# Performance work log

Hardware: AMD Instinct MI355X
Metric: run time of the kernel (lower is better)

The kernel has to match this reference:

```python
import jax, jax.numpy as jnp
import numpy as np

NUM_LAYERS = 3
NUM_NODES = 120000  # num_users + num_items
LATENT_DIM = 64
NUM_EDGES = 2000000


def setup_inputs() -> dict:
    key = jax.random.key(0)
    k1, k2 = jax.random.split(key)
    edge_index = jax.random.randint(k1, (2, NUM_EDGES), 0, NUM_NODES, dtype=jnp.int64 if jax.config.jax_enable_x64 else jnp.int32)
    # init_parameters: normal(std=0.1) for LightGCN
    emb_weight = jax.random.normal(k2, (NUM_NODES, LATENT_DIM), dtype=jnp.float32) * 0.1
    return {"edge_index": edge_index, "emb_weight": emb_weight}


def reference(edge_index, emb_weight):
    """RecSysGNN (model='LightGCN') forward. Returns (emb0, out)."""
    n = emb_weight.shape[0]
    src, dst = edge_index[0], edge_index[1]
    # degree of target nodes (degree(to_, x.size(0)))
    deg = jax.ops.segment_sum(jnp.ones(src.shape[0], dtype=emb_weight.dtype), dst, num_segments=n)
    deg_inv_sqrt = jnp.where(deg > 0, jax.lax.rsqrt(jnp.maximum(deg, 1.0)), 0.0)
    norm = deg_inv_sqrt[src] * deg_inv_sqrt[dst]  # [E]

    emb0 = emb_weight
    emb = emb0
    acc = emb0  # running sum of layer embeddings for final mean
    for _ in range(NUM_LAYERS):
        msg = norm[:, None] * emb[src]                      # [E, d] gather + scale
        emb = jax.ops.segment_sum(msg, dst, num_segments=n)  # scatter-add to targets
        acc = acc + emb
    out = acc / (NUM_LAYERS + 1)  # mean over stacked [emb0, emb1, ..., embL]
    return (emb0, out)
```

## Files before the change

kernel.cpp:

```cpp
#include <hip/hip_runtime.h>


#define DIM 64
#define BN 512
#define BSH 9
#define CHUNK 4096

typedef unsigned short u16;
typedef unsigned int u32;

static __device__ __forceinline__ float bf2f_lo(u32 p) { return __uint_as_float(p << 16); }
static __device__ __forceinline__ float bf2f_hi(u32 p) { return __uint_as_float(p & 0xffff0000u); }
static __device__ __forceinline__ u16 f2bf(float f) {
    unsigned u = __float_as_uint(f);
    return (u16)((u + 0x7fffu + ((u >> 16) & 1u)) >> 16);
}
static __device__ __forceinline__ u32 pack2(float a, float b) {
    return (u32)f2bf(a) | ((u32)f2bf(b) << 16);
}

__global__ void zero_cur(int* __restrict__ cursor) { cursor[threadIdx.x] = 0; }

__global__ void __launch_bounds__(512) c1_scatter(
        const int* __restrict__ src, const int* __restrict__ dst,
        int* __restrict__ cursor, u32* __restrict__ slab, int E, int CAP) {
    __shared__ u32 buf[CHUNK];
    __shared__ unsigned char bb[CHUNK];
    __shared__ int posb[256], startb[256], gbase[256];
    int w = blockIdx.x, tid = threadIdx.x;
    int lo = w * CHUNK, hi = min(lo + CHUNK, E);
    if (tid < 256) posb[tid] = 0;
    __syncthreads();
    for (int i = lo + tid; i < hi; i += 512) atomicAdd(&posb[dst[i] >> BSH], 1);
    __syncthreads();
    int x = 0;
    if (tid < 256) {
        x = posb[tid];
        gbase[tid] = x ? atomicAdd(cursor + tid, x) : 0;
    }
    __syncthreads();
    for (int off = 1; off < 256; off <<= 1) {
        int t = (tid >= off && tid < 256) ? posb[tid - off] : 0;
        __syncthreads();
        if (tid < 256) posb[tid] += t;
        __syncthreads();
    }
    if (tid < 256) startb[tid] = posb[tid] - x;
    __syncthreads();
    if (tid < 256) posb[tid] = startb[tid];
    __syncthreads();
    for (int i = lo + tid; i < hi; i += 512) {
        int d = dst[i], b = d >> BSH;
        int q = atomicAdd(&posb[b], 1);
        buf[q] = ((u32)src[i] << BSH) | (u32)(d & (BN - 1));
        bb[q] = (unsigned char)b;
    }
    __syncthreads();
    int n = hi - lo;
    for (int q = tid; q < n; q += 512) {
        int b = bb[q];
        slab[(size_t)b * CAP + gbase[b] + (q - startb[b])] = buf[q];
    }
}

__global__ void __launch_bounds__(512) c3_build(
        const u32* __restrict__ slab, const int* __restrict__ cursor,
        int* __restrict__ col, int2* __restrict__ row_se, float* __restrict__ dis,
        int N, int CAP, int NB) {
    __shared__ int cur[BN];
    __shared__ int ps[512];
    int b = blockIdx.x, tid = threadIdx.x;
    int xc = (tid < NB) ? cursor[tid] : 0;
    if (tid < 256) ps[tid] = xc;
    __syncthreads();
    for (int off = 1; off < 256; off <<= 1) {
        int t = (tid >= off && tid < 256) ? ps[tid - off] : 0;
        __syncthreads();
        if (tid < 256) ps[tid] += t;
        __syncthreads();
    }
    int lo  = b ? ps[b - 1] : 0;
    int cnt = cursor[b];
    __syncthreads();

    int nodeBase = b << BSH;
    int nLoc = min(BN, N - nodeBase);
    const u32* sp = slab + (size_t)b * CAP;
    cur[tid] = 0;
    __syncthreads();
    for (int i = tid; i < cnt; i += 512) atomicAdd(&cur[sp[i] & (BN - 1)], 1);
    __syncthreads();
    int c0 = cur[tid];
    ps[tid] = c0;
    __syncthreads();
    for (int off = 1; off < 512; off <<= 1) {
        int t = (tid >= off) ? ps[tid - off] : 0;
        __syncthreads();
        ps[tid] += t;
        __syncthreads();
    }
    int base = ps[tid] - c0;
    cur[tid] = base;
    if (tid < nLoc) {
        dis[nodeBase + tid] = c0 ? rsqrtf((float)c0) : 0.f;
        row_se[nodeBase + tid] = make_int2(lo + base, lo + base + c0);
    }
    __syncthreads();
    for (int i = tid; i < cnt; i += 512) {
        u32 v = sp[i];
        int q = atomicAdd(&cur[v & (BN - 1)], 1);
        col[lo + q] = (int)(v >> BSH);
    }
}

__global__ void cvt_copy(const float4* __restrict__ emb, const float* __restrict__ dis,
                         ushort4* __restrict__ e0b, float4* __restrict__ emb0_out, int n4) {
    int i = blockIdx.x * blockDim.x + threadIdx.x;
    if (i < n4) {
        float4 v = emb[i];
        float w = dis[i >> 4];
        ushort4 o;
        o.x = f2bf(w * v.x); o.y = f2bf(w * v.y);
        o.z = f2bf(w * v.z); o.w = f2bf(w * v.w);
        e0b[i] = o;
        emb0_out[i] = v;
    }
}

#define ACC4(P) { s0 += bf2f_lo((P).x); s1 += bf2f_hi((P).x);                  \
                  s2 += bf2f_lo((P).y); s3 += bf2f_hi((P).y); }

#define GATHER_BODY(CURTAB)                                                    \
    float s0 = 0.f, s1 = 0.f, s2 = 0.f, s3 = 0.f;                              \
    {                                                                          \
        int nfull = (end - start) >> 3;                                        \
        uint2 p0, p1, p2, p3;                                                  \
        if (nfull > 0) {                                                       \
            int j = start;                                                     \
            int a0 = col[j + g],     a1 = col[j + 2 + g];                      \
            int a2 = col[j + 4 + g], a3 = col[j + 6 + g];                      \
            p0 = *(const uint2*)((CURTAB) + (((size_t)a0) << 5) + 2 * d);      \
            p1 = *(const uint2*)((CURTAB) + (((size_t)a1) << 5) + 2 * d);      \
            p2 = *(const uint2*)((CURTAB) + (((size_t)a2) << 5) + 2 * d);      \
            p3 = *(const uint2*)((CURTAB) + (((size_t)a3) << 5) + 2 * d);      \
        }                                                                      \
        for (int r = 1; r < nfull; ++r) {                                      \
            int jn = start + 8 * r;                                            \
            int b0 = col[jn + g],     b1 = col[jn + 2 + g];                    \
            int b2 = col[jn + 4 + g], b3 = col[jn + 6 + g];                    \
            uint2 q0 = *(const uint2*)((CURTAB) + (((size_t)b0) << 5) + 2 * d);\
            uint2 q1 = *(const uint2*)((CURTAB) + (((size_t)b1) << 5) + 2 * d);\
            uint2 q2 = *(const uint2*)((CURTAB) + (((size_t)b2) << 5) + 2 * d);\
            uint2 q3 = *(const uint2*)((CURTAB) + (((size_t)b3) << 5) + 2 * d);\
            ACC4(p0) ACC4(p1) ACC4(p2) ACC4(p3)                                \
            p0 = q0; p1 = q1; p2 = q2; p3 = q3;                                \
        }                                                                      \
        if (nfull > 0) { ACC4(p0) ACC4(p1) ACC4(p2) ACC4(p3) }                 \
        int jt = start + 8 * nfull;                                            \
        if (jt < end) {                                                        \
            int endm1 = end - 1;                                               \
            _Pragma("unroll")                                                  \
            for (int k = 0; k < 4; ++k) {                                      \
                int e = jt + 2 * k + g;                                        \
                int c = col[min(e, endm1)];                                    \
                uint2 p = *(const uint2*)((CURTAB) + (((size_t)c) << 5) + 2 * d); \
                if (e >= end) { p.x = 0; p.y = 0; }                            \
                ACC4(p)                                                        \
            }                                                                  \
        }                                                                      \
    }                                                                          \
    s0 += __shfl_xor(s0, 16); s1 += __shfl_xor(s1, 16);                        \
    s2 += __shfl_xor(s2, 16); s3 += __shfl_xor(s3, 16);

__global__ void __launch_bounds__(256) gather_mid(
        const int2* __restrict__ row_se, const int* __restrict__ col,
        const float* __restrict__ dis, const u32* __restrict__ cur,
        u32* __restrict__ next, int N) {
    int t = blockIdx.x * blockDim.x + threadIdx.x;
    int pair = t >> 6, lane = t & 63;
    if (2 * pair >= N) return;
    int node = 2 * pair + (lane >> 5);
    int g = (lane >> 4) & 1, d = lane & 15;
    bool valid = node < N;
    int2 se = valid ? row_se[node] : make_int2(0, 0);
    int start = se.x, end = se.y;
    GATHER_BODY(cur)
    if (valid && g == 0) {
        float w = dis[node], ww = w * w;
        uint2 o;
        o.x = pack2(ww * s0, ww * s1);
        o.y = pack2(ww * s2, ww * s3);
        *(uint2*)(next + (((size_t)node) << 5) + 2 * d) = o;
    }
}

__global__ void __launch_bounds__(256) gather_final(
        const int2* __restrict__ row_se, const int* __restrict__ col,
        const float* __restrict__ dis, const u32* __restrict__ cur ,
        const u32* __restrict__ e1b, const float* __restrict__ emb0,
        float* __restrict__ out, int N) {
    int t = blockIdx.x * blockDim.x + threadIdx.x;
    int pair = t >> 6, lane = t & 63;
    if (2 * pair >= N) return;
    int node = 2 * pair + (lane >> 5);
    int g = (lane >> 4) & 1, d = lane & 15;
    bool valid = node < N;
    int2 se = valid ? row_se[node] : make_int2(0, 0);
    int start = se.x, end = se.y;
    GATHER_BODY(cur)
    if (valid && g == 0) {
        float w = dis[node];
        float inv = (w > 0.f) ? 1.0f / w : 0.f;
        size_t idx = (((size_t)node) << 5) + 2 * d;
        uint2 q1 = *(const uint2*)(e1b + idx);
        uint2 q2 = *(const uint2*)(cur + idx);
        float4 e0 = *(const float4*)(emb0 + 2 * idx);
        float4 r;
        r.x = 0.25f * (e0.x + (bf2f_lo(q1.x) + bf2f_lo(q2.x)) * inv + w * s0);
        r.y = 0.25f * (e0.y + (bf2f_hi(q1.x) + bf2f_hi(q2.x)) * inv + w * s1);
        r.z = 0.25f * (e0.z + (bf2f_lo(q1.y) + bf2f_lo(q2.y)) * inv + w * s2);
        r.w = 0.25f * (e0.w + (bf2f_hi(q1.y) + bf2f_hi(q2.y)) * inv + w * s3);
        *(float4*)(out + 2 * idx) = r;
    }
}

extern "C" void kernel_launch(void* const* d_in, const int* in_sizes, int n_in,
                              void* d_out, int out_size, void* d_ws, size_t ws_size,
                              hipStream_t stream) {
    const int*   edge  = (const int*)d_in[0];
    const float* emb_w = (const float*)d_in[1];
    const int E = in_sizes[0] / 2;
    const int N = in_sizes[1] / DIM;
    const int* src = edge;
    const int* dst = edge + E;

    const int NB  = (N + BN - 1) >> BSH;
    const int nCh = (E + CHUNK - 1) / CHUNK;
    const int CAP = (E / (NB > 0 ? NB : 1)) * 2;

    float* out_base = (float*)d_out;
    float* emb0_out = out_base;
    float* acc      = out_base + (size_t)N * DIM;

    float* dis       = (float*)d_ws;
    int2*  row_se    = (int2*)(dis + ((N + 1) & ~1));
    int*   cursor    = (int*)(row_se + N);
    int*   col       = cursor + 256;
    u32*   slab      = (u32*)(col + E);
    u16*   e0b       = (u16*)slab;
    u16*   e1b       = e0b + (size_t)N * DIM;

    const int n4    = N * DIM / 4;
    const int BLK   = 256;
    const int g4    = (n4 + BLK - 1) / BLK;
    const int PAIRS = (N + 1) / 2;
    const int gW    = (PAIRS * 64 + BLK - 1) / BLK;

    zero_cur<<<1, 256, 0, stream>>>(cursor);
    c1_scatter<<<nCh, 512, 0, stream>>>(src, dst, cursor, slab, E, CAP);
    c3_build<<<NB, 512, 0, stream>>>(slab, cursor, col, row_se, dis, N, CAP, NB);

    cvt_copy<<<g4, BLK, 0, stream>>>((const float4*)emb_w, dis,
                                     (ushort4*)e0b, (float4*)emb0_out, n4);

    gather_mid<<<gW, BLK, 0, stream>>>(row_se, col, dis, (const u32*)e0b, (u32*)e1b, N);
    gather_mid<<<gW, BLK, 0, stream>>>(row_se, col, dis, (const u32*)e1b, (u32*)e0b, N);
    gather_final<<<gW, BLK, 0, stream>>>(row_se, col, dis, (const u32*)e0b, (const u32*)e1b,
                                         emb_w, acc, N);
}
```

Before: 256.6 us.

## Split CSR rows into padded half-lists for vectorized column loads

The CSR build now stores each node's neighbour list as two interleaved halves, each padded to a multiple of four with zeros. This lets each half-wave in the gather read four column indices with a single 16-byte load instead of scalar strided loads. The layer-1 bf16 buffer is also moved into the output accumulator region with a 64-word row stride, freeing workspace, and gather_final reads it in place before overwriting it. The padding enlarges the col array and the build kernel does extra zero-filling work.

```diff
diff --git a/kernel.cpp b/kernel.cpp
--- a/kernel.cpp
+++ b/kernel.cpp
@@ -5,6 +5,7 @@
 #define BN 512
 #define BSH 9
 #define CHUNK 4096
+#define PADB 4096
 
 typedef unsigned short u16;
 typedef unsigned int u32;
@@ -68,6 +69,8 @@
         int* __restrict__ col, int2* __restrict__ row_se, float* __restrict__ dis,
         int N, int CAP, int NB) {
     __shared__ int cur[BN];
+    __shared__ int sAv[BN];
+    __shared__ int pAv[BN];
     __shared__ int ps[512];
     int b = blockIdx.x, tid = threadIdx.x;
     int xc = (tid < NB) ? cursor[tid] : 0;
@@ -79,9 +82,10 @@
         if (tid < 256) ps[tid] += t;
         __syncthreads();
     }
-    int lo  = b ? ps[b - 1] : 0;
+    int lo_raw = b ? ps[b - 1] : 0;
     int cnt = cursor[b];
     __syncthreads();
+    int lo_pad = ((lo_raw + 3) & ~3) + b * PADB;
 
     int nodeBase = b << BSH;
     int nLoc = min(BN, N - nodeBase);
@@ -91,7 +95,10 @@
     for (int i = tid; i < cnt; i += 512) atomicAdd(&cur[sp[i] & (BN - 1)], 1);
     __syncthreads();
     int c0 = cur[tid];
-    ps[tid] = c0;
+    int cA = (c0 + 1) >> 1, cB = c0 >> 1;
+    int padA = (cA + 3) & ~3;
+    int padn = padA + ((cB + 3) & ~3);
+    ps[tid] = padn;
     __syncthreads();
     for (int off = 1; off < 512; off <<= 1) {
         int t = (tid >= off) ? ps[tid - off] : 0;
@@ -99,17 +106,24 @@
         ps[tid] += t;
         __syncthreads();
     }
-    int base = ps[tid] - c0;
-    cur[tid] = base;
+    int sA = lo_pad + ps[tid] - padn;
+    __syncthreads();
+    cur[tid] = 0;
+    sAv[tid] = sA; pAv[tid] = padA;
     if (tid < nLoc) {
         dis[nodeBase + tid] = c0 ? rsqrtf((float)c0) : 0.f;
-        row_se[nodeBase + tid] = make_int2(lo + base, lo + base + c0);
-    }
+        row_se[nodeBase + tid] = make_int2(sA, c0);
+    }
+    for (int p = cA; p < padA; ++p) col[sA + p] = 0;
+    int sB = sA + padA, padBn = padn - padA;
+    for (int p = cB; p < padBn; ++p) col[sB + p] = 0;
     __syncthreads();
     for (int i = tid; i < cnt; i += 512) {
         u32 v = sp[i];
-        int q = atomicAdd(&cur[v & (BN - 1)], 1);
-        col[lo + q] = (int)(v >> BSH);
+        int ln = v & (BN - 1);
+        int p = atomicAdd(&cur[ln], 1);
+        int t = sAv[ln] + ((p & 1) ? pAv[ln] + (p >> 1) : (p >> 1));
+        col[t] = (int)(v >> BSH);
     }
 }
 
@@ -129,49 +143,44 @@
 
 #define ACC4(P) { s0 += bf2f_lo((P).x); s1 += bf2f_hi((P).x);                  \
                   s2 += bf2f_lo((P).y); s3 += bf2f_hi((P).y); }
-
-#define GATHER_BODY(CURTAB)                                                    \
+#define ROWLD(CI) (*(const uint2*)((CURTAB) + (((size_t)(u32)(CI)) << (SH)) + 2 * d))
+
+#define GATHERQ(CURTAB, SH)                                                    \
     float s0 = 0.f, s1 = 0.f, s2 = 0.f, s3 = 0.f;                              \
     {                                                                          \
-        int nfull = (end - start) >> 3;                                        \
+        int cAq  = (c + 1) >> 1;                                               \
+        int padA = (cAq + 3) & ~3;                                             \
+        int mg   = g ? (c >> 1) : cAq;                                         \
+        const int* cp = col + sA + (g ? padA : 0);                             \
+        int nfull = mg >> 2;                                                   \
         uint2 p0, p1, p2, p3;                                                  \
         if (nfull > 0) {                                                       \
-            int j = start;                                                     \
-            int a0 = col[j + g],     a1 = col[j + 2 + g];                      \
-            int a2 = col[j + 4 + g], a3 = col[j + 6 + g];                      \
-            p0 = *(const uint2*)((CURTAB) + (((size_t)a0) << 5) + 2 * d);      \
-            p1 = *(const uint2*)((CURTAB) + (((size_t)a1) << 5) + 2 * d);      \
-            p2 = *(const uint2*)((CURTAB) + (((size_t)a2) << 5) + 2 * d);      \
-            p3 = *(const uint2*)((CURTAB) + (((size_t)a3) << 5) + 2 * d);      \
+            uint4 cv = *(const uint4*)cp;                                      \
+            p0 = ROWLD(cv.x); p1 = ROWLD(cv.y);                                \
+            p2 = ROWLD(cv.z); p3 = ROWLD(cv.w);                                \
         }                                                                      \
         for (int r = 1; r < nfull; ++r) {                                      \
-            int jn = start + 8 * r;                                            \
-            int b0 = col[jn + g],     b1 = col[jn + 2 + g];                    \
-            int b2 = col[jn + 4 + g], b3 = col[jn + 6 + g];                    \
-            uint2 q0 = *(const uint2*)((CURTAB) + (((size_t)b0) << 5) + 2 * d);\
-            uint2 q1 = *(const uint2*)((CURTAB) + (((size_t)b1) << 5) + 2 * d);\
-            uint2 q2 = *(const uint2*)((CURTAB) + (((size_t)b2) << 5) + 2 * d);\
-            uint2 q3 = *(const uint2*)((CURTAB) + (((size_t)b3) << 5) + 2 * d);\
+            uint4 cv = *(const uint4*)(cp + 4 * r);                            \
+            uint2 q0 = ROWLD(cv.x), q1 = ROWLD(cv.y);                          \
+            uint2 q2 = ROWLD(cv.z), q3 = ROWLD(cv.w);                          \
             ACC4(p0) ACC4(p1) ACC4(p2) ACC4(p3)                                \
             p0 = q0; p1 = q1; p2 = q2; p3 = q3;                                \
         }                                                                      \
         if (nfull > 0) { ACC4(p0) ACC4(p1) ACC4(p2) ACC4(p3) }                 \
-        int jt = start + 8 * nfull;                                            \
-        if (jt < end) {                                                        \
-            int endm1 = end - 1;                                               \
-            _Pragma("unroll")                                                  \
-            for (int k = 0; k < 4; ++k) {                                      \
-                int e = jt + 2 * k + g;                                        \
-                int c = col[min(e, endm1)];                                    \
-                uint2 p = *(const uint2*)((CURTAB) + (((size_t)c) << 5) + 2 * d); \
-                if (e >= end) { p.x = 0; p.y = 0; }                            \
-                ACC4(p)                                                        \
-            }                                                                  \
+        int t0 = nfull << 2;                                                   \
+        if (t0 < mg) {                                                         \
+            uint4 cv = *(const uint4*)(cp + t0);                               \
+            uint2 pk;                                                          \
+            pk = ROWLD(cv.x); if (t0 + 0 >= mg) { pk.x = 0; pk.y = 0; } ACC4(pk) \
+            pk = ROWLD(cv.y); if (t0 + 1 >= mg) { pk.x = 0; pk.y = 0; } ACC4(pk) \
+            pk = ROWLD(cv.z); if (t0 + 2 >= mg) { pk.x = 0; pk.y = 0; } ACC4(pk) \
+            pk = ROWLD(cv.w); if (t0 + 3 >= mg) { pk.x = 0; pk.y = 0; } ACC4(pk) \
         }                                                                      \
     }                                                                          \
     s0 += __shfl_xor(s0, 16); s1 += __shfl_xor(s1, 16);                        \
     s2 += __shfl_xor(s2, 16); s3 += __shfl_xor(s3, 16);
 
+template<int INSH, int OUTSH>
 __global__ void __launch_bounds__(256) gather_mid(
         const int2* __restrict__ row_se, const int* __restrict__ col,
         const float* __restrict__ dis, const u32* __restrict__ cur,
@@ -183,22 +192,23 @@
     int g = (lane >> 4) & 1, d = lane & 15;
     bool valid = node < N;
     int2 se = valid ? row_se[node] : make_int2(0, 0);
-    int start = se.x, end = se.y;
-    GATHER_BODY(cur)
+    int sA = se.x, c = se.y;
+    const u32* CURTAB = cur; constexpr int SH = INSH;
+    GATHERQ(CURTAB, SH)
     if (valid && g == 0) {
         float w = dis[node], ww = w * w;
         uint2 o;
         o.x = pack2(ww * s0, ww * s1);
         o.y = pack2(ww * s2, ww * s3);
-        *(uint2*)(next + (((size_t)node) << 5) + 2 * d) = o;
+        *(uint2*)(next + (((size_t)node) << OUTSH) + 2 * d) = o;
     }
 }
 
 __global__ void __launch_bounds__(256) gather_final(
         const int2* __restrict__ row_se, const int* __restrict__ col,
         const float* __restrict__ dis, const u32* __restrict__ cur ,
-        const u32* __restrict__ e1b, const float* __restrict__ emb0,
-        float* __restrict__ out, int N) {
+        const u32* e1b, const float* __restrict__ emb0,
+        float* out, int N) {
     int t = blockIdx.x * blockDim.x + threadIdx.x;
     int pair = t >> 6, lane = t & 63;
     if (2 * pair >= N) return;
@@ -206,21 +216,22 @@
     int g = (lane >> 4) & 1, d = lane & 15;
     bool valid = node < N;
     int2 se = valid ? row_se[node] : make_int2(0, 0);
-    int start = se.x, end = se.y;
-    GATHER_BODY(cur)
+    int sA = se.x, c = se.y;
+    const u32* CURTAB = cur; constexpr int SH = 5;
+    GATHERQ(CURTAB, SH)
     if (valid && g == 0) {
         float w = dis[node];
         float inv = (w > 0.f) ? 1.0f / w : 0.f;
-        size_t idx = (((size_t)node) << 5) + 2 * d;
-        uint2 q1 = *(const uint2*)(e1b + idx);
-        uint2 q2 = *(const uint2*)(cur + idx);
-        float4 e0 = *(const float4*)(emb0 + 2 * idx);
+        uint2 q1 = *(const uint2*)(e1b + ((size_t)node << 6) + 2 * d);
+        uint2 q2 = *(const uint2*)(cur + ((size_t)node << 5) + 2 * d);
+        size_t fo = (size_t)node * 64 + 4 * d;
+        float4 e0 = *(const float4*)(emb0 + fo);
         float4 r;
         r.x = 0.25f * (e0.x + (bf2f_lo(q1.x) + bf2f_lo(q2.x)) * inv + w * s0);
         r.y = 0.25f * (e0.y + (bf2f_hi(q1.x) + bf2f_hi(q2.x)) * inv + w * s1);
         r.z = 0.25f * (e0.z + (bf2f_lo(q1.y) + bf2f_lo(q2.y)) * inv + w * s2);
         r.w = 0.25f * (e0.w + (bf2f_hi(q1.y) + bf2f_hi(q2.y)) * inv + w * s3);
-        *(float4*)(out + 2 * idx) = r;
+        *(float4*)(out + fo) = r;
     }
 }
 
@@ -241,17 +252,18 @@
     float* out_base = (float*)d_out;
     float* emb0_out = out_base;
     float* acc      = out_base + (size_t)N * DIM;
+    u32*   e1b      = (u32*)acc;
 
     float* dis       = (float*)d_ws;
     int2*  row_se    = (int2*)(dis + ((N + 1) & ~1));
     int*   cursor    = (int*)(row_se + N);
     int*   col       = cursor + 256;
-    u32*   slab      = (u32*)(col + E);
-    u16*   e0b       = (u16*)slab;
-    u16*   e1b       = e0b + (size_t)N * DIM;
-
+    const int COLSZ  = E + NB * PADB + 64;
+    u32*   slab      = (u32*)(col + COLSZ);
+    u32*   e0b       = slab;
+
+    const int BLK   = 256;
     const int n4    = N * DIM / 4;
-    const int BLK   = 256;
     const int g4    = (n4 + BLK - 1) / BLK;
     const int PAIRS = (N + 1) / 2;
     const int gW    = (PAIRS * 64 + BLK - 1) / BLK;
@@ -263,8 +275,8 @@
     cvt_copy<<<g4, BLK, 0, stream>>>((const float4*)emb_w, dis,
                                      (ushort4*)e0b, (float4*)emb0_out, n4);
 
-    gather_mid<<<gW, BLK, 0, stream>>>(row_se, col, dis, (const u32*)e0b, (u32*)e1b, N);
-    gather_mid<<<gW, BLK, 0, stream>>>(row_se, col, dis, (const u32*)e1b, (u32*)e0b, N);
-    gather_final<<<gW, BLK, 0, stream>>>(row_se, col, dis, (const u32*)e0b, (const u32*)e1b,
+    gather_mid<5, 6><<<gW, BLK, 0, stream>>>(row_se, col, dis, e0b, e1b, N);
+    gather_mid<6, 5><<<gW, BLK, 0, stream>>>(row_se, col, dis, e1b, e0b, N);
+    gather_final<<<gW, BLK, 0, stream>>>(row_se, col, dis, e0b, e1b,
                                          emb_w, acc, N);
 }
```

Result: slower. 262.0 us (+2.1%).

## Build CSR via global degree atomics and direct placement instead of bucketed slab

Applied to the files above, without the earlier changes.

Replaces the two-pass bucketed slab CSR construction with a degree histogram from global atomics, per-block sums, a prefix-scan kernel that sets row offsets and cursors, and a placement kernel that writes each source into col through an atomic cursor. The layer-1 bf16 buffer now lives in the output accumulator region with a 64-word row stride, which saves workspace. Global atomics on 2M edges can contend and leave the order of edges within each row nondeterministic. That hurts locality and makes the float sums order-dependent, in exchange for fewer passes and no slab.

```diff
diff --git a/kernel.cpp b/kernel.cpp
--- a/kernel.cpp
+++ b/kernel.cpp
@@ -4,7 +4,6 @@
 #define DIM 64
 #define BN 512
 #define BSH 9
-#define CHUNK 4096
 
 typedef unsigned short u16;
 typedef unsigned int u32;
@@ -19,58 +18,43 @@
     return (u32)f2bf(a) | ((u32)f2bf(b) << 16);
 }
 
-__global__ void zero_cur(int* __restrict__ cursor) { cursor[threadIdx.x] = 0; }
-
-__global__ void __launch_bounds__(512) c1_scatter(
-        const int* __restrict__ src, const int* __restrict__ dst,
-        int* __restrict__ cursor, u32* __restrict__ slab, int E, int CAP) {
-    __shared__ u32 buf[CHUNK];
-    __shared__ unsigned char bb[CHUNK];
-    __shared__ int posb[256], startb[256], gbase[256];
-    int w = blockIdx.x, tid = threadIdx.x;
-    int lo = w * CHUNK, hi = min(lo + CHUNK, E);
-    if (tid < 256) posb[tid] = 0;
-    __syncthreads();
-    for (int i = lo + tid; i < hi; i += 512) atomicAdd(&posb[dst[i] >> BSH], 1);
-    __syncthreads();
-    int x = 0;
-    if (tid < 256) {
-        x = posb[tid];
-        gbase[tid] = x ? atomicAdd(cursor + tid, x) : 0;
-    }
-    __syncthreads();
-    for (int off = 1; off < 256; off <<= 1) {
-        int t = (tid >= off && tid < 256) ? posb[tid - off] : 0;
-        __syncthreads();
-        if (tid < 256) posb[tid] += t;
-        __syncthreads();
-    }
-    if (tid < 256) startb[tid] = posb[tid] - x;
-    __syncthreads();
-    if (tid < 256) posb[tid] = startb[tid];
-    __syncthreads();
-    for (int i = lo + tid; i < hi; i += 512) {
-        int d = dst[i], b = d >> BSH;
-        int q = atomicAdd(&posb[b], 1);
-        buf[q] = ((u32)src[i] << BSH) | (u32)(d & (BN - 1));
-        bb[q] = (unsigned char)b;
-    }
-    __syncthreads();
-    int n = hi - lo;
-    for (int q = tid; q < n; q += 512) {
-        int b = bb[q];
-        slab[(size_t)b * CAP + gbase[b] + (q - startb[b])] = buf[q];
-    }
-}
-
-__global__ void __launch_bounds__(512) c3_build(
-        const u32* __restrict__ slab, const int* __restrict__ cursor,
-        int* __restrict__ col, int2* __restrict__ row_se, float* __restrict__ dis,
-        int N, int CAP, int NB) {
-    __shared__ int cur[BN];
+__global__ void __launch_bounds__(256) k_deg(
+        const int* __restrict__ dst, int* __restrict__ deg, int E) {
+    int i = (blockIdx.x * 256 + threadIdx.x) * 4;
+    if (i + 3 < E) {
+        int4 d = *(const int4*)(dst + i);
+        atomicAdd(&deg[d.x], 1); atomicAdd(&deg[d.y], 1);
+        atomicAdd(&deg[d.z], 1); atomicAdd(&deg[d.w], 1);
+    } else {
+        for (; i < E; ++i) atomicAdd(&deg[dst[i]], 1);
+    }
+}
+
+__global__ void __launch_bounds__(128) k_bsum(
+        const int* __restrict__ deg, int* __restrict__ btot, int N) {
+    __shared__ int s[128];
+    int b = blockIdx.x, t = threadIdx.x;
+    int base = b << BSH;
+    int sum = 0;
+    for (int k = t; k < BN; k += 128) {
+        int n = base + k;
+        sum += (n < N) ? deg[n] : 0;
+    }
+    s[t] = sum; __syncthreads();
+    for (int off = 64; off > 0; off >>= 1) {
+        if (t < off) s[t] += s[t + off];
+        __syncthreads();
+    }
+    if (t == 0) btot[b] = s[0];
+}
+
+__global__ void __launch_bounds__(512) c3_fin(
+        const int* __restrict__ deg, const int* __restrict__ btot,
+        int2* __restrict__ row_se, float* __restrict__ dis,
+        int* __restrict__ cursor, int N, int NB) {
     __shared__ int ps[512];
     int b = blockIdx.x, tid = threadIdx.x;
-    int xc = (tid < NB) ? cursor[tid] : 0;
+    int xc = (tid < NB) ? btot[tid] : 0;
     if (tid < 256) ps[tid] = xc;
     __syncthreads();
     for (int off = 1; off < 256; off <<= 1) {
@@ -79,18 +63,10 @@
         if (tid < 256) ps[tid] += t;
         __syncthreads();
     }
-    int lo  = b ? ps[b - 1] : 0;
-    int cnt = cursor[b];
+    int lo = b ? ps[b - 1] : 0;
     __syncthreads();
-
-    int nodeBase = b << BSH;
-    int nLoc = min(BN, N - nodeBase);
-    const u32* sp = slab + (size_t)b * CAP;
-    cur[tid] = 0;
-    __syncthreads();
-    for (int i = tid; i < cnt; i += 512) atomicAdd(&cur[sp[i] & (BN - 1)], 1);
-    __syncthreads();
-    int c0 = cur[tid];
+    int node = (b << BSH) + tid;
+    int c0 = (node < N) ? deg[node] : 0;
     ps[tid] = c0;
     __syncthreads();
     for (int off = 1; off < 512; off <<= 1) {
@@ -99,17 +75,27 @@
         ps[tid] += t;
         __syncthreads();
     }
-    int base = ps[tid] - c0;
-    cur[tid] = base;
-    if (tid < nLoc) {
-        dis[nodeBase + tid] = c0 ? rsqrtf((float)c0) : 0.f;
-        row_se[nodeBase + tid] = make_int2(lo + base, lo + base + c0);
-    }
-    __syncthreads();
-    for (int i = tid; i < cnt; i += 512) {
-        u32 v = sp[i];
-        int q = atomicAdd(&cur[v & (BN - 1)], 1);
-        col[lo + q] = (int)(v >> BSH);
+    int start = lo + ps[tid] - c0;
+    if (node < N) {
+        dis[node] = c0 ? rsqrtf((float)c0) : 0.f;
+        row_se[node] = make_int2(start, start + c0);
+        cursor[node] = start;
+    }
+}
+
+__global__ void __launch_bounds__(256) k_place(
+        const int* __restrict__ src, const int* __restrict__ dst,
+        int* __restrict__ cursor, int* __restrict__ col, int E) {
+    int i = (blockIdx.x * 256 + threadIdx.x) * 4;
+    if (i + 3 < E) {
+        int4 s = *(const int4*)(src + i);
+        int4 d = *(const int4*)(dst + i);
+        col[atomicAdd(&cursor[d.x], 1)] = s.x;
+        col[atomicAdd(&cursor[d.y], 1)] = s.y;
+        col[atomicAdd(&cursor[d.z], 1)] = s.z;
+        col[atomicAdd(&cursor[d.w], 1)] = s.w;
+    } else {
+        for (; i < E; ++i) col[atomicAdd(&cursor[dst[i]], 1)] = src[i];
     }
 }
 
@@ -130,7 +116,7 @@
 #define ACC4(P) { s0 += bf2f_lo((P).x); s1 += bf2f_hi((P).x);                  \
                   s2 += bf2f_lo((P).y); s3 += bf2f_hi((P).y); }
 
-#define GATHER_BODY(CURTAB)                                                    \
+#define GATHER_BODY(CURTAB, SH)                                                \
     float s0 = 0.f, s1 = 0.f, s2 = 0.f, s3 = 0.f;                              \
     {                                                                          \
         int nfull = (end - start) >> 3;                                        \
@@ -139,19 +125,19 @@
             int j = start;                                                     \
             int a0 = col[j + g],     a1 = col[j + 2 + g];                      \
             int a2 = col[j + 4 + g], a3 = col[j + 6 + g];                      \
-            p0 = *(const uint2*)((CURTAB) + (((size_t)a0) << 5) + 2 * d);      \
-            p1 = *(const uint2*)((CURTAB) + (((size_t)a1) << 5) + 2 * d);      \
-            p2 = *(const uint2*)((CURTAB) + (((size_t)a2) << 5) + 2 * d);      \
-            p3 = *(const uint2*)((CURTAB) + (((size_t)a3) << 5) + 2 * d);      \
+            p0 = *(const uint2*)((CURTAB) + (((size_t)a0) << (SH)) + 2 * d);   \
+            p1 = *(const uint2*)((CURTAB) + (((size_t)a1) << (SH)) + 2 * d);   \
+            p2 = *(const uint2*)((CURTAB) + (((size_t)a2) << (SH)) + 2 * d);   \
+            p3 = *(const uint2*)((CURTAB) + (((size_t)a3) << (SH)) + 2 * d);   \
         }                                                                      \
         for (int r = 1; r < nfull; ++r) {                                      \
             int jn = start + 8 * r;                                            \
             int b0 = col[jn + g],     b1 = col[jn + 2 + g];                    \
             int b2 = col[jn + 4 + g], b3 = col[jn + 6 + g];                    \
-            uint2 q0 = *(const uint2*)((CURTAB) + (((size_t)b0) << 5) + 2 * d);\
-            uint2 q1 = *(const uint2*)((CURTAB) + (((size_t)b1) << 5) + 2 * d);\
-            uint2 q2 = *(const uint2*)((CURTAB) + (((size_t)b2) << 5) + 2 * d);\
-            uint2 q3 = *(const uint2*)((CURTAB) + (((size_t)b3) << 5) + 2 * d);\
+            uint2 q0 = *(const uint2*)((CURTAB) + (((size_t)b0) << (SH)) + 2 * d); \
+            uint2 q1 = *(const uint2*)((CURTAB) + (((size_t)b1) << (SH)) + 2 * d); \
+            uint2 q2 = *(const uint2*)((CURTAB) + (((size_t)b2) << (SH)) + 2 * d); \
+            uint2 q3 = *(const uint2*)((CURTAB) + (((size_t)b3) << (SH)) + 2 * d); \
             ACC4(p0) ACC4(p1) ACC4(p2) ACC4(p3)                                \
             p0 = q0; p1 = q1; p2 = q2; p3 = q3;                                \
         }                                                                      \
@@ -163,7 +149,7 @@
             for (int k = 0; k < 4; ++k) {                                      \
                 int e = jt + 2 * k + g;                                        \
                 int c = col[min(e, endm1)];                                    \
-                uint2 p = *(const uint2*)((CURTAB) + (((size_t)c) << 5) + 2 * d); \
+                uint2 p = *(const uint2*)((CURTAB) + (((size_t)c) << (SH)) + 2 * d); \
                 if (e >= end) { p.x = 0; p.y = 0; }                            \
                 ACC4(p)                                                        \
             }                                                                  \
@@ -172,6 +158,7 @@
     s0 += __shfl_xor(s0, 16); s1 += __shfl_xor(s1, 16);                        \
     s2 += __shfl_xor(s2, 16); s3 += __shfl_xor(s3, 16);
 
+template<int INSH, int OUTSH>
 __global__ void __launch_bounds__(256) gather_mid(
         const int2* __restrict__ row_se, const int* __restrict__ col,
         const float* __restrict__ dis, const u32* __restrict__ cur,
@@ -184,21 +171,21 @@
     bool valid = node < N;
     int2 se = valid ? row_se[node] : make_int2(0, 0);
     int start = se.x, end = se.y;
-    GATHER_BODY(cur)
+    GATHER_BODY(cur, INSH)
     if (valid && g == 0) {
         float w = dis[node], ww = w * w;
         uint2 o;
         o.x = pack2(ww * s0, ww * s1);
         o.y = pack2(ww * s2, ww * s3);
-        *(uint2*)(next + (((size_t)node) << 5) + 2 * d) = o;
+        *(uint2*)(next + (((size_t)node) << OUTSH) + 2 * d) = o;
     }
 }
 
 __global__ void __launch_bounds__(256) gather_final(
         const int2* __restrict__ row_se, const int* __restrict__ col,
         const float* __restrict__ dis, const u32* __restrict__ cur ,
-        const u32* __restrict__ e1b, const float* __restrict__ emb0,
-        float* __restrict__ out, int N) {
+        const u32* e1b, const float* __restrict__ emb0,
+        float* out, int N) {
     int t = blockIdx.x * blockDim.x + threadIdx.x;
     int pair = t >> 6, lane = t & 63;
     if (2 * pair >= N) return;
@@ -207,20 +194,20 @@
     bool valid = node < N;
     int2 se = valid ? row_se[node] : make_int2(0, 0);
     int start = se.x, end = se.y;
-    GATHER_BODY(cur)
+    GATHER_BODY(cur, 5)
     if (valid && g == 0) {
         float w = dis[node];
         float inv = (w > 0.f) ? 1.0f / w : 0.f;
-        size_t idx = (((size_t)node) << 5) + 2 * d;
-        uint2 q1 = *(const uint2*)(e1b + idx);
-        uint2 q2 = *(const uint2*)(cur + idx);
-        float4 e0 = *(const float4*)(emb0 + 2 * idx);
+        uint2 q1 = *(const uint2*)(e1b + ((size_t)node << 6) + 2 * d);
+        uint2 q2 = *(const uint2*)(cur + ((size_t)node << 5) + 2 * d);
+        size_t fo = (size_t)node * 64 + 4 * d;
+        float4 e0 = *(const float4*)(emb0 + fo);
         float4 r;
         r.x = 0.25f * (e0.x + (bf2f_lo(q1.x) + bf2f_lo(q2.x)) * inv + w * s0);
         r.y = 0.25f * (e0.y + (bf2f_hi(q1.x) + bf2f_hi(q2.x)) * inv + w * s1);
         r.z = 0.25f * (e0.z + (bf2f_lo(q1.y) + bf2f_lo(q2.y)) * inv + w * s2);
         r.w = 0.25f * (e0.w + (bf2f_hi(q1.y) + bf2f_hi(q2.y)) * inv + w * s3);
-        *(float4*)(out + 2 * idx) = r;
+        *(float4*)(out + fo) = r;
     }
 }
 
@@ -234,37 +221,39 @@
     const int* src = edge;
     const int* dst = edge + E;
 
-    const int NB  = (N + BN - 1) >> BSH;
-    const int nCh = (E + CHUNK - 1) / CHUNK;
-    const int CAP = (E / (NB > 0 ? NB : 1)) * 2;
+    const int NB = (N + BN - 1) >> BSH;
 
     float* out_base = (float*)d_out;
     float* emb0_out = out_base;
     float* acc      = out_base + (size_t)N * DIM;
-
-    float* dis       = (float*)d_ws;
-    int2*  row_se    = (int2*)(dis + ((N + 1) & ~1));
-    int*   cursor    = (int*)(row_se + N);
-    int*   col       = cursor + 256;
-    u32*   slab      = (u32*)(col + E);
-    u16*   e0b       = (u16*)slab;
-    u16*   e1b       = e0b + (size_t)N * DIM;
-
+    u32*   e1b      = (u32*)acc;
+
+    float* dis    = (float*)d_ws;
+    int2*  row_se = (int2*)(dis + ((N + 3) & ~3));
+    int*   deg    = (int*)(row_se + N);
+    int*   cursor = deg + ((N + 3) & ~3);
+    int*   btot   = cursor + ((N + 3) & ~3);
+    int*   col    = btot + 256;
+    u32*   e0b    = (u32*)(col + ((E + 3) & ~3));
+
+    const int BLK   = 256;
     const int n4    = N * DIM / 4;
-    const int BLK   = 256;
     const int g4    = (n4 + BLK - 1) / BLK;
+    const int gE    = (E + BLK * 4 - 1) / (BLK * 4);
     const int PAIRS = (N + 1) / 2;
     const int gW    = (PAIRS * 64 + BLK - 1) / BLK;
 
-    zero_cur<<<1, 256, 0, stream>>>(cursor);
-    c1_scatter<<<nCh, 512, 0, stream>>>(src, dst, cursor, slab, E, CAP);
-    c3_build<<<NB, 512, 0, stream>>>(slab, cursor, col, row_se, dis, N, CAP, NB);
+    hipMemsetAsync(deg, 0, (size_t)N * sizeof(int), stream);
+    k_deg<<<gE, BLK, 0, stream>>>(dst, deg, E);
+    k_bsum<<<NB, 128, 0, stream>>>(deg, btot, N);
+    c3_fin<<<NB, 512, 0, stream>>>(deg, btot, row_se, dis, cursor, N, NB);
+    k_place<<<gE, BLK, 0, stream>>>(src, dst, cursor, col, E);
 
     cvt_copy<<<g4, BLK, 0, stream>>>((const float4*)emb_w, dis,
                                      (ushort4*)e0b, (float4*)emb0_out, n4);
 
-    gather_mid<<<gW, BLK, 0, stream>>>(row_se, col, dis, (const u32*)e0b, (u32*)e1b, N);
-    gather_mid<<<gW, BLK, 0, stream>>>(row_se, col, dis, (const u32*)e1b, (u32*)e0b, N);
-    gather_final<<<gW, BLK, 0, stream>>>(row_se, col, dis, (const u32*)e0b, (const u32*)e1b,
+    gather_mid<5, 6><<<gW, BLK, 0, stream>>>(row_se, col, dis, e0b, e1b, N);
+    gather_mid<6, 5><<<gW, BLK, 0, stream>>>(row_se, col, dis, e1b, e0b, N);
+    gather_final<<<gW, BLK, 0, stream>>>(row_se, col, dis, e0b, e1b,
                                          emb_w, acc, N);
 }
```

Result: slower. 474.7 us (+85.0%).
